# Kernel tuning notes

Hardware: AMD Instinct MI355X
Metric: run time of the kernel (lower is better)

Reference implementation:

```python
import jax, jax.numpy as jnp
from jax import lax
import numpy as np

DEPTH = 4
D_MODEL = 192
D_INNER = 384
D_STATE = 16
D_CONV = 4
DT_RANK = 12
STRIDE = 4
NUM_PATCHES = 400
L_SEQ = NUM_PATCHES + 1  # +1 cls token appended at the end
EPS = 1e-5


def _rmsnorm(x, w):
    x = x.astype(jnp.float32)
    return (x * lax.rsqrt(jnp.mean(x * x, axis=-1, keepdims=True) + EPS)) * w


def _mamba(x, in_w, cw, cb, xp_w, dtw, dtb, A_log, Dv, ow):
    # x: [B, L, D_MODEL]
    B = x.shape[0]
    xz = jnp.einsum('bld,ed->ble', x, in_w)            # [B, L, 2*D_INNER]
    u, z = jnp.split(xz, 2, axis=-1)                   # [B, L, D_INNER] each
    # causal depthwise conv over L
    u_t = jnp.transpose(u, (0, 2, 1))                  # [B, D_INNER, L]
    u_pad = jnp.pad(u_t, ((0, 0), (0, 0), (D_CONV - 1, 0)))
    conv = lax.conv_general_dilated(
        u_pad, cw[:, None, :], (1,), 'VALID',
        dimension_numbers=('NCH', 'OIH', 'NCH'),
        feature_group_count=D_INNER)                   # [B, D_INNER, L]
    u = jax.nn.silu(conv + cb[:, None])
    u = jnp.transpose(u, (0, 2, 1))                    # [B, L, D_INNER]
    xdbl = jnp.einsum('bld,ed->ble', u, xp_w)          # [B, L, 44]
    dt, Bm, Cm = jnp.split(xdbl, [DT_RANK, DT_RANK + D_STATE], axis=-1)
    dt = jax.nn.softplus(jnp.einsum('blr,dr->bld', dt, dtw) + dtb)  # [B, L, D_INNER]
    A = -jnp.exp(A_log)                                # [D_INNER, D_STATE]
    dA = jnp.exp(dt[..., None] * A)                    # [B, L, D_INNER, D_STATE]
    dBu = dt[..., None] * Bm[:, :, None, :] * u[..., None]
    h0 = jnp.zeros((B, D_INNER, D_STATE), dtype=dA.dtype)

    def step(h, inp):
        dA_t, dBu_t = inp
        h = dA_t * h + dBu_t
        return h, h

    _, hs = lax.scan(step, h0, (jnp.swapaxes(dA, 0, 1), jnp.swapaxes(dBu, 0, 1)))
    hs = jnp.swapaxes(hs, 0, 1)                        # [B, L, D_INNER, D_STATE]
    y = jnp.einsum('bldn,bln->bld', hs, Cm) + u * Dv
    y = y * jax.nn.silu(z)
    return jnp.einsum('bld,ed->ble', y, ow)            # [B, L, D_MODEL]


def _forward(imgs, patch_w, patch_b, pos_embed, cls_token, norm_w, in_proj_w,
             conv_w, conv_b, xproj_w, dt_w, dt_b, A_log, D_param, out_w,
             normf_w, head_w, head_b):
    B = imgs.shape[0]
    # StrideEmbed: non-overlapping strides of 4 bytes -> linear to embed_dim
    x = imgs.reshape(B, NUM_PATCHES, STRIDE) @ patch_w + patch_b  # [B, 400, 192]
    x = x + pos_embed[:, :-1, :]
    cls = cls_token + pos_embed[:, -1:, :]             # [1, 1, 192]
    x = jnp.concatenate([x, jnp.broadcast_to(cls, (B, 1, D_MODEL))], axis=1)
    hidden = x
    residual = None
    for i in range(DEPTH):
        residual = hidden if residual is None else hidden + residual  # fp32 residual stream
        h = _rmsnorm(residual, norm_w[i])
        hidden = _mamba(h, in_proj_w[i], conv_w[i], conv_b[i], xproj_w[i],
                        dt_w[i], dt_b[i], A_log[i], D_param[i], out_w[i])
    x = _rmsnorm(hidden + residual, normf_w)
    cls_out = x[:, -1, :]                              # [B, 192]
    logits = cls_out @ head_w.T + head_b               # [B, 1000]
    return logits


def setup_inputs() -> dict:
    key = jax.random.key(0)
    ks = jax.random.split(key, 16)
    B = 32
    rn = lambda k, s, sc: jax.random.normal(k, s, dtype=jnp.float32) * sc
    A_log = jnp.broadcast_to(jnp.log(jnp.arange(1.0, D_STATE + 1.0, dtype=jnp.float32)),
                             (DEPTH, D_INNER, D_STATE))
    return {
        'imgs': rn(ks[0], (B, 1, 40, 40), 1.0),
        'patch_w': rn(ks[1], (STRIDE, D_MODEL), 0.1),
        'patch_b': jnp.zeros((D_MODEL,), jnp.float32),
        'pos_embed': rn(ks[2], (1, L_SEQ, D_MODEL), 0.02),
        'cls_token': rn(ks[3], (1, 1, D_MODEL), 0.02),
        'norm_w': jnp.ones((DEPTH, D_MODEL), jnp.float32),
        'in_proj_w': rn(ks[4], (DEPTH, 2 * D_INNER, D_MODEL), 0.05),
        'conv_w': rn(ks[5], (DEPTH, D_INNER, D_CONV), 0.3),
        'conv_b': jnp.zeros((DEPTH, D_INNER), jnp.float32),
        'xproj_w': rn(ks[6], (DEPTH, DT_RANK + 2 * D_STATE, D_INNER), 0.05),
        'dt_w': rn(ks[7], (DEPTH, D_INNER, DT_RANK), 0.1),
        'dt_b': rn(ks[8], (DEPTH, D_INNER), 0.5) - 4.0,
        'A_log': A_log,
        'D_param': jnp.ones((DEPTH, D_INNER), jnp.float32),
        'out_w': rn(ks[9], (DEPTH, D_MODEL, D_INNER), 0.05),
        'normf_w': jnp.ones((D_MODEL,), jnp.float32),
        'head_w': rn(ks[10], (1000, D_MODEL), 0.05),
        'head_b': jnp.zeros((1000,), jnp.float32),
    }


def reference(imgs, patch_w, patch_b, pos_embed, cls_token, norm_w, in_proj_w,
              conv_w, conv_b, xproj_w, dt_w, dt_b, A_log, D_param, out_w,
              normf_w, head_w, head_b):
    return _forward(imgs, patch_w, patch_b, pos_embed, cls_token, norm_w,
                    in_proj_w, conv_w, conv_b, xproj_w, dt_w, dt_b, A_log,
                    D_param, out_w, normf_w, head_w, head_b)
```

## Files before the change

### kernel.cpp

```cpp
#include <hip/hip_runtime.h>
#include <hip/hip_bf16.h>

#define B_SZ 32
#define LSEQ 401
#define NT (B_SZ * LSEQ)
#define DM 192
#define DI 384
#define DS 16
#define EPSF 1e-5f
#define ST 40
#define STP 44
#define NCH 8
#define PQN 1376256

typedef __attribute__((ext_vector_type(8))) short short8;
typedef __attribute__((ext_vector_type(4))) float f32x4;
typedef __hip_bfloat16 bf16;

#define OFF_IMGS    0
#define OFF_PATCHW  51200
#define OFF_PATCHB  51968
#define OFF_POS     52160
#define OFF_CLS     129152
#define OFF_NORMW   129344
#define OFF_INW     130112
#define OFF_CONVW   719936
#define OFF_CONVB   726080
#define OFF_XPROJW  727616
#define OFF_DTW     795200
#define OFF_DTB     813632
#define OFF_ALOG    815168
#define OFF_DP      839744
#define OFF_OUTW    841280
#define OFF_NORMF   1136192
#define OFF_HEADW   1136384
#define OFF_HEADB   1328384
#define OFF_TOTAL   1329384

#define WB_INW   0
#define WB_XPJ   589824
#define WB_OUT   688128
#define WB_DTW   983040
#define WB_TOTAL 1032192

__device__ __forceinline__ int chunk_s(int c) { return c == 0 ? 0 : c * 50 + 1; }
__device__ __forceinline__ int chunk_e(int c) { return (c + 1) * 50 + 1; }

__device__ __forceinline__ float ldsrc(const void* p, int off, int isbf) {
  return isbf ? __bfloat162float(((const bf16*)p)[off]) : ((const float*)p)[off];
}
__device__ __forceinline__ float fast_silu(float z) {
  return z * __builtin_amdgcn_rcpf(1.f + __expf(-z));
}
__device__ __forceinline__ float fast_softplus(float x) {
  float e = __expf(x);
  return (x > 15.f) ? x : __logf(1.f + e);
}

#define DPP_ADD(x, ctrl) \
  x += __int_as_float(__builtin_amdgcn_update_dpp(0, __float_as_int(x), ctrl, 0xF, 0xF, true))
__device__ __forceinline__ float row_sum16(float x) {
  DPP_ADD(x, 0xB1);
  DPP_ADD(x, 0x4E);
  DPP_ADD(x, 0x124);
  DPP_ADD(x, 0x128);
  return x;
}

struct P18 { const void* p[18]; };

__global__ __launch_bounds__(256) void k_convwb(P18 t, float* __restrict__ fin,
                                                bf16* __restrict__ wb) {
  static const int st[19] = {OFF_IMGS, OFF_PATCHW, OFF_PATCHB, OFF_POS, OFF_CLS,
                             OFF_NORMW, OFF_INW, OFF_CONVW, OFF_CONVB, OFF_XPROJW,
                             OFF_DTW, OFF_DTB, OFF_ALOG, OFF_DP, OFF_OUTW,
                             OFF_NORMF, OFF_HEADW, OFF_HEADB, OFF_TOTAL};
  int isbf = (((const unsigned short*)t.p[5])[0] == 0x3F80) ? 1 : 0;
  int idx = blockIdx.x * 256 + threadIdx.x;
  if (idx < OFF_TOTAL) {
    int lo = 0;
#pragma unroll
    for (int i = 1; i < 18; ++i) if (idx >= st[i]) lo = i;
    fin[idx] = ldsrc(t.p[lo], idx - st[lo], isbf);
  } else if (idx < OFF_TOTAL + WB_TOTAL) {
    int j = idx - OFF_TOTAL;
    float v;
    if (j < WB_XPJ) {
      v = ldsrc(t.p[6], j, isbf);
    } else if (j < WB_OUT) {
      int i2 = j - WB_XPJ;
      int l = i2 / (64 * 384);
      int r = (i2 / 384) & 63;
      int k = i2 % 384;
      v = (r < 44) ? ldsrc(t.p[9], l * 44 * 384 + r * 384 + k, isbf) : 0.f;
    } else if (j < WB_DTW) {
      v = ldsrc(t.p[14], j - WB_OUT, isbf);
    } else {
      int i2 = j - WB_DTW;
      int l = i2 / (384 * 32);
      int r = i2 % (384 * 32);
      int d = r >> 5;
      int k = r & 31;
      v = (k < 12) ? ldsrc(t.p[10], l * 4608 + d * 12 + k, isbf) : 0.f;
    }
    wb[j] = __float2bfloat16(v);
  }
}

__device__ __forceinline__ void inproj32(const bf16 (*shb)[200],
                                         const bf16* __restrict__ Win,
                                         bf16* __restrict__ xb,
                                         bf16* __restrict__ zb,
                                         int row0, int tid) {
  int lane = tid & 63, wave = tid >> 6;
  int q = lane >> 4, mlo = lane & 15;
  short8 afrA[6], afrB[6];
#pragma unroll
  for (int kk = 0; kk < 6; ++kk) {
    afrA[kk] = *(const short8*)&shb[mlo][kk * 32 + q * 8];
    afrB[kk] = *(const short8*)&shb[16 + mlo][kk * 32 + q * 8];
  }
  const bf16* wbase = Win + (size_t)(wave * 96 + mlo) * DM + q * 8;
#pragma unroll
  for (int jh = 0; jh < 2; ++jh) {
    short8 Bb[18];
#pragma unroll
    for (int j = 0; j < 3; ++j)
#pragma unroll
      for (int kk = 0; kk < 6; ++kk)
        Bb[j * 6 + kk] = *(const short8*)(wbase + (size_t)(jh * 3 + j) * 16 * DM + kk * 32);
#pragma unroll
    for (int j = 0; j < 3; ++j) {
      f32x4 aA = {}, aB = {};
#pragma unroll
      for (int kk = 0; kk < 6; ++kk) {
        aA = __builtin_amdgcn_mfma_f32_16x16x32_bf16(afrA[kk], Bb[j * 6 + kk], aA, 0, 0, 0);
        aB = __builtin_amdgcn_mfma_f32_16x16x32_bf16(afrB[kk], Bb[j * 6 + kk], aB, 0, 0, 0);
      }
      int n = wave * 96 + (jh * 3 + j) * 16 + mlo;
      if (n < DI) {
#pragma unroll
        for (int i = 0; i < 4; ++i) {
          xb[(size_t)(row0 + q * 4 + i) * DI + n] = __float2bfloat16(aA[i]);
          xb[(size_t)(row0 + 16 + q * 4 + i) * DI + n] = __float2bfloat16(aB[i]);
        }
      } else {
        int nz = n - DI;
#pragma unroll
        for (int i = 0; i < 4; ++i) {
          zb[(size_t)(row0 + q * 4 + i) * DI + nz] = __float2bfloat16(aA[i]);
          zb[(size_t)(row0 + 16 + q * 4 + i) * DI + nz] = __float2bfloat16(aB[i]);
        }
      }
    }
  }
}

__global__ __launch_bounds__(512)
__attribute__((amdgpu_waves_per_eu(2, 2)))
void k_embedin(const float* __restrict__ fin,
               float* __restrict__ residual,
               const bf16* __restrict__ Win,
               bf16* __restrict__ xb,
               bf16* __restrict__ zb) {
  __shared__ bf16 shb[32][200];
  const float* imgs = fin + OFF_IMGS;
  const float* pw   = fin + OFF_PATCHW;
  const float* pb   = fin + OFF_PATCHB;
  const float* pos  = fin + OFF_POS;
  const float* cls  = fin + OFF_CLS;
  const float* nw0  = fin + OFF_NORMW;
  int tid = threadIdx.x;
  int row0 = blockIdx.x * 32;
  {
    int row = tid >> 4, g = tid & 15;
    int t = row0 + row;
    int b = t / LSEQ, l = t % LSEQ;
    float im[4];
    if (l < 400) {
#pragma unroll
      for (int s = 0; s < 4; ++s) im[s] = imgs[b * 1600 + l * 4 + s];
    }
    float rn[12], ss = 0.f;
#pragma unroll
    for (int k = 0; k < 12; ++k) {
      int col = g + 16 * k;
      float v;
      if (l < 400) {
        v = pb[col] + pos[l * DM + col];
#pragma unroll
        for (int s = 0; s < 4; ++s) v = fmaf(im[s], pw[s * DM + col], v);
      } else {
        v = cls[col] + pos[400 * DM + col];
      }
      residual[(size_t)t * DM + col] = v;
      rn[k] = v;
      ss = fmaf(v, v, ss);
    }
    ss = row_sum16(ss);
    float sres = rsqrtf(ss / (float)DM + EPSF);
#pragma unroll
    for (int k = 0; k < 12; ++k) {
      int col = g + 16 * k;
      shb[row][col] = __float2bfloat16(rn[k] * sres * nw0[col]);
    }
  }
  __syncthreads();
  inproj32(shb, Win, xb, zb, row0, tid);
}

__global__ __launch_bounds__(512) void k_xdt(const bf16* __restrict__ xb,
                                             const float* __restrict__ cw,
                                             const float* __restrict__ cb,
                                             const bf16* __restrict__ Wbf,
                                             float* __restrict__ xdbl,
                                             const bf16* __restrict__ dtwb,
                                             const float* __restrict__ dtb,
                                             bf16* __restrict__ ub,
                                             bf16* __restrict__ dto) {
  __shared__ bf16  sxt[19][392];
  __shared__ bf16  su[16][392];
  __shared__ float4 scw4[384];
  __shared__ float scb[384];
  __shared__ float sxp[2][16][48];
  __shared__ bf16  sxb[16][32];
  int row0 = blockIdx.x * 16;
  int tid = threadIdx.x;
  for (int i = tid; i < 19 * 48; i += 512) {
    int r = i / 48, c8 = i - r * 48;
    int t = row0 - 3 + r;
    if (t < 0) t = 0;
    *(short8*)&sxt[r][c8 * 8] = *(const short8*)(xb + (size_t)t * DI + c8 * 8);
  }
  for (int i = tid; i < 384; i += 512) {
    scw4[i] = ((const float4*)cw)[i];
    scb[i] = cb[i];
  }
  __syncthreads();
  for (int i = tid; i < 768; i += 512) {
    int tok = i / 48;
    int c8 = i - tok * 48;
    int d0 = c8 * 8;
    int t = row0 + tok;
    int l = t % LSEQ;
    float xr[4][8];
#pragma unroll
    for (int k = 0; k < 4; ++k) {
      short8 v = *(const short8*)&sxt[tok + k][d0];
      bool ok = (l - 3 + k) >= 0;
#pragma unroll
      for (int j = 0; j < 8; ++j) {
        unsigned int uu = ((unsigned int)(unsigned short)v[j]) << 16;
        xr[k][j] = ok ? __uint_as_float(uu) : 0.f;
      }
    }
    short8 uvv;
#pragma unroll
    for (int j = 0; j < 8; ++j) {
      float4 w = scw4[d0 + j];
      float a = scb[d0 + j];
      a = fmaf(xr[0][j], w.x, a);
      a = fmaf(xr[1][j], w.y, a);
      a = fmaf(xr[2][j], w.z, a);
      a = fmaf(xr[3][j], w.w, a);
      bf16 h = __float2bfloat16(fast_silu(a));
      uvv[j] = *reinterpret_cast<short*>(&h);
    }
    *(short8*)&su[tok][d0] = uvv;
    *(short8*)(ub + (size_t)t * DI + d0) = uvv;
  }
  __syncthreads();
  int lane = tid & 63;
  int wave = tid >> 6;
  int q = lane >> 4;
  int mlo = lane & 15;
  if (wave < 6) {
    int colw = (wave % 3) * 16;
    int kh = wave / 3;
    f32x4 acc = {};
    for (int k0 = 0; k0 < 192; k0 += 32) {
      short8 a = *(const short8*)&su[mlo][kh * 192 + k0 + q * 8];
      short8 b = *(const short8*)(Wbf + (size_t)(colw + mlo) * DI + kh * 192 + k0 + q * 8);
      acc = __builtin_amdgcn_mfma_f32_16x16x32_bf16(a, b, acc, 0, 0, 0);
    }
#pragma unroll
    for (int i = 0; i < 4; ++i) sxp[kh][q * 4 + i][colw + mlo] = acc[i];
  }
  __syncthreads();
  for (int i = tid; i < 16 * 44; i += 512) {
    int r = i / 44, c = i - r * 44;
    xdbl[(size_t)(row0 + r) * 44 + c] = sxp[0][r][c] + sxp[1][r][c];
  }
  for (int i = tid; i < 512; i += 512) {
    int tok = i >> 5, k = i & 31;
    sxb[tok][k] = __float2bfloat16(k < 12 ? sxp[0][tok][k] + sxp[1][tok][k] : 0.f);
  }
  __syncthreads();
  short8 afrag = *(const short8*)&sxb[mlo][q * 8];
#pragma unroll
  for (int jt = 0; jt < 3; ++jt) {
    int d = (wave * 3 + jt) * 16 + mlo;
    short8 bfrag = *(const short8*)(dtwb + (size_t)d * 32 + q * 8);
    f32x4 acc = {};
    acc = __builtin_amdgcn_mfma_f32_16x16x32_bf16(afrag, bfrag, acc, 0, 0, 0);
    float dtbv = dtb[d];
#pragma unroll
    for (int i = 0; i < 4; ++i)
      dto[(size_t)(row0 + q * 4 + i) * DI + d] =
          __float2bfloat16(fast_softplus(acc[i] + dtbv));
  }
}

__global__ __launch_bounds__(512) void k_scanA(const bf16* __restrict__ ub,
                                               const bf16* __restrict__ dtv,
                                               const float* __restrict__ xdbl,
                                               const float* __restrict__ A_log,
                                               float* __restrict__ Pq) {
  __shared__ float sdt[32][STP], sw[32][STP], sB[16][STP];
  int bx = blockIdx.x, b = blockIdx.y, c = blockIdx.z;
  int d0 = bx * 32;
  int tid = threadIdx.x;
  int dloc = tid >> 4, n = tid & 15;
  float A = -__expf(A_log[(d0 + dloc) * DS + n]);
  float S = 0.f, h = 0.f;
  int base = b * LSEQ;
  int lt = tid >> 5, lj = tid & 31;
  int s = chunk_s(c), e = chunk_e(c);
  for (int t0 = s; t0 < e; t0 += ST) {
    int tc = min(ST, e - t0);
    for (int tt = lt; tt < tc; tt += 16) {
      int g = base + t0 + tt;
      float dv = __bfloat162float(dtv[(size_t)g * DI + d0 + lj]);
      sdt[lj][tt] = dv;
      sw[lj][tt] = dv * __bfloat162float(ub[(size_t)g * DI + d0 + lj]);
      if (lj < 16) sB[lj][tt] = xdbl[(size_t)g * 44 + 12 + lj];
    }
    __syncthreads();
    int l4 = 0;
    for (; l4 + 4 <= tc; l4 += 4) {
      float4 dt4 = *(const float4*)&sdt[dloc][l4];
      float4 w4  = *(const float4*)&sw[dloc][l4];
      float4 B4  = *(const float4*)&sB[n][l4];
      h = fmaf(__expf(dt4.x * A), h, w4.x * B4.x);
      h = fmaf(__expf(dt4.y * A), h, w4.y * B4.y);
      h = fmaf(__expf(dt4.z * A), h, w4.z * B4.z);
      h = fmaf(__expf(dt4.w * A), h, w4.w * B4.w);
      S += dt4.x + dt4.y + dt4.z + dt4.w;
    }
    for (; l4 < tc; ++l4) {
      float dv = sdt[dloc][l4];
      h = fmaf(__expf(dv * A), h, sw[dloc][l4] * sB[n][l4]);
      S += dv;
    }
    __syncthreads();
  }
  int idx = ((c * B_SZ + b) * 12 + bx) * 512 + tid;
  Pq[idx] = __expf(A * S);
  Pq[PQN + idx] = h;
}

__global__ __launch_bounds__(512) void k_scanB(const bf16* __restrict__ zb,
                                               const bf16* __restrict__ ub,
                                               const bf16* __restrict__ dtv,
                                               const float* __restrict__ xdbl,
                                               const float* __restrict__ A_log,
                                               const float* __restrict__ Dp,
                                               const float* __restrict__ Pq,
                                               bf16* __restrict__ yb) {
  __shared__ float sdt[32][STP], sw[32][STP], sB[16][STP], sC[16][STP],
                   sz[32][STP], sy[32][STP];
  int bx = blockIdx.x, b = blockIdx.y, c = blockIdx.z;
  int d0 = bx * 32;
  int tid = threadIdx.x;
  int dloc = tid >> 4, n = tid & 15;
  float A = -__expf(A_log[(d0 + dloc) * DS + n]);
  float h = 0.f;
  for (int j = 0; j < c; ++j) {
    int idx = ((j * B_SZ + b) * 12 + bx) * 512 + tid;
    h = Pq[PQN + idx] + Pq[idx] * h;
  }
  int base = b * LSEQ;
  int lt = tid >> 5, lj = tid & 31;
  float Dvj = Dp[d0 + lj];
  int s = chunk_s(c), e = chunk_e(c);
  for (int t0 = s; t0 < e; t0 += ST) {
    int tc = min(ST, e - t0);
    for (int tt = lt; tt < tc; tt += 16) {
      int g = base + t0 + tt;
      float dv = __bfloat162float(dtv[(size_t)g * DI + d0 + lj]);
      float uv = __bfloat162float(ub[(size_t)g * DI + d0 + lj]);
      sdt[lj][tt] = dv;
      sw[lj][tt] = dv * uv;
      sy[lj][tt] = uv * Dvj;
      sz[lj][tt] = fast_silu(__bfloat162float(zb[(size_t)g * DI + d0 + lj]));
      if (lj < 32) {
        float v = xdbl[(size_t)g * 44 + 12 + lj];
        if (lj < 16) sB[lj][tt] = v;
        else         sC[lj - 16][tt] = v;
      }
    }
    __syncthreads();
    int l4 = 0;
    for (; l4 + 4 <= tc; l4 += 4) {
      float4 dt4 = *(const float4*)&sdt[dloc][l4];
      float4 w4  = *(const float4*)&sw[dloc][l4];
      float4 B4  = *(const float4*)&sB[n][l4];
      float4 C4  = *(const float4*)&sC[n][l4];
      float c0, c1, c2, c3;
      h = fmaf(__expf(dt4.x * A), h, w4.x * B4.x); c0 = row_sum16(h * C4.x);
      h = fmaf(__expf(dt4.y * A), h, w4.y * B4.y); c1 = row_sum16(h * C4.y);
      h = fmaf(__expf(dt4.z * A), h, w4.z * B4.z); c2 = row_sum16(h * C4.z);
      h = fmaf(__expf(dt4.w * A), h, w4.w * B4.w); c3 = row_sum16(h * C4.w);
      if (n == 0) {
        float4 uD4 = *(const float4*)&sy[dloc][l4];
        float4 z4  = *(const float4*)&sz[dloc][l4];
        float4 yv;
        yv.x = (c0 + uD4.x) * z4.x;
        yv.y = (c1 + uD4.y) * z4.y;
        yv.z = (c2 + uD4.z) * z4.z;
        yv.w = (c3 + uD4.w) * z4.w;
        *(float4*)&sy[dloc][l4] = yv;
      }
    }
    for (; l4 < tc; ++l4) {
      h = fmaf(__expf(sdt[dloc][l4] * A), h, sw[dloc][l4] * sB[n][l4]);
      float cc = row_sum16(h * sC[n][l4]);
      if (n == 0) sy[dloc][l4] = (cc + sy[dloc][l4]) * sz[dloc][l4];
    }
    __syncthreads();
    for (int tt = lt; tt < tc; tt += 16)
      yb[(size_t)(base + t0 + tt) * DI + d0 + lj] = __float2bfloat16(sy[lj][tt]);
    __syncthreads();
  }
}

__global__ __launch_bounds__(512)
__attribute__((amdgpu_waves_per_eu(2, 2)))
void k_outin(const bf16* __restrict__ yb,
             const bf16* __restrict__ Wout,
             float* __restrict__ residual,
             const float* __restrict__ nw,
             const bf16* __restrict__ Win,
             bf16* __restrict__ xb,
             bf16* __restrict__ zb) {
  __shared__ bf16  syt[32][392];
  __shared__ float sCt[2][32][200];
  __shared__ bf16  shb[32][200];
  int tid = threadIdx.x;
  int lane = tid & 63;
  int wave = tid >> 6;
  int row0 = blockIdx.x * 32;
  int q = lane >> 4;
  int mlo = lane & 15;
  {
    int i0 = tid, i1 = tid + 512, i2 = tid + 1024;
    const bf16* src = yb + (size_t)row0 * DI;
    short8 v0 = *(const short8*)(src + (i0 / 48) * DI + (i0 % 48) * 8);
    short8 v1 = *(const short8*)(src + (i1 / 48) * DI + (i1 % 48) * 8);
    short8 v2 = *(const short8*)(src + (i2 / 48) * DI + (i2 % 48) * 8);
    *(short8*)&syt[i0 / 48][(i0 % 48) * 8] = v0;
    *(short8*)&syt[i1 / 48][(i1 % 48) * 8] = v1;
    *(short8*)&syt[i2 / 48][(i2 % 48) * 8] = v2;
  }
  __syncthreads();
  {
    int colw = (wave & 3) * 48;
    int kh = wave >> 2;
    const bf16* brow = Wout + (size_t)(colw + mlo) * DI + kh * 192 + q * 8;
    short8 Bf[18];
#pragma unroll
    for (int j = 0; j < 3; ++j)
#pragma unroll
      for (int k2 = 0; k2 < 6; ++k2)
        Bf[j * 6 + k2] = *(const short8*)(brow + (size_t)j * 16 * DI + k2 * 32);
    short8 afA[6], afB[6];
#pragma unroll
    for (int k2 = 0; k2 < 6; ++k2) {
      afA[k2] = *(const short8*)&syt[mlo][kh * 192 + k2 * 32 + q * 8];
      afB[k2] = *(const short8*)&syt[16 + mlo][kh * 192 + k2 * 32 + q * 8];
    }
    f32x4 acc[2][3] = {};
#pragma unroll
    for (int k2 = 0; k2 < 6; ++k2) {
#pragma unroll
      for (int j = 0; j < 3; ++j) {
        acc[0][j] = __builtin_amdgcn_mfma_f32_16x16x32_bf16(afA[k2], Bf[j * 6 + k2], acc[0][j], 0, 0, 0);
        acc[1][j] = __builtin_amdgcn_mfma_f32_16x16x32_bf16(afB[k2], Bf[j * 6 + k2], acc[1][j], 0, 0, 0);
      }
    }
#pragma unroll
    for (int rg = 0; rg < 2; ++rg)
#pragma unroll
      for (int j = 0; j < 3; ++j)
#pragma unroll
        for (int i = 0; i < 4; ++i)
          sCt[kh][rg * 16 + q * 4 + i][colw + j * 16 + mlo] = acc[rg][j][i];
  }
  __syncthreads();
  {
    int row = tid >> 4, g = tid & 15;
    int t = row0 + row;
    float* rp = residual + (size_t)t * DM + g * 12;
    float4 r4[3];
#pragma unroll
    for (int j = 0; j < 3; ++j) r4[j] = *(const float4*)(rp + j * 4);
    float rn[12], ss = 0.f;
#pragma unroll
    for (int k = 0; k < 12; ++k) {
      int col = g * 12 + k;
      float x = sCt[0][row][col] + sCt[1][row][col] + ((const float*)r4)[k];
      rn[k] = x;
      ss = fmaf(x, x, ss);
    }
    ss = row_sum16(ss);
    float sres = rsqrtf(ss / (float)DM + EPSF);
#pragma unroll
    for (int j = 0; j < 3; ++j) {
      float4 w4;
      w4.x = rn[j * 4 + 0]; w4.y = rn[j * 4 + 1];
      w4.z = rn[j * 4 + 2]; w4.w = rn[j * 4 + 3];
      *(float4*)(rp + j * 4) = w4;
    }
#pragma unroll
    for (int k = 0; k < 12; ++k) {
      int col = g * 12 + k;
      shb[row][col] = __float2bfloat16(rn[k] * sres * nw[col]);
    }
  }
  __syncthreads();
  inproj32(shb, Win, xb, zb, row0, tid);
}

__global__ __launch_bounds__(256) void k_lastout(const bf16* __restrict__ yb,
                                                 const bf16* __restrict__ Wout,
                                                 const float* __restrict__ resIn,
                                                 float* __restrict__ clsbuf) {
  __shared__ float sCt[16][200];
  int tid = threadIdx.x;
  int lane = tid & 63;
  int wave = tid >> 6;
  int b0 = blockIdx.x * 16;
  int q = lane >> 4;
  int mlo = lane & 15;
  int colw = wave * 48;
  f32x4 acc[3] = {};
  const bf16* arow = yb + ((size_t)(b0 + mlo) * LSEQ + 400) * DI + q * 8;
  for (int k0 = 0; k0 < DI; k0 += 32) {
    short8 a = *(const short8*)(arow + k0);
#pragma unroll
    for (int j = 0; j < 3; ++j) {
      short8 b = *(const short8*)(Wout + (size_t)(colw + j * 16 + mlo) * DI + k0 + q * 8);
      acc[j] = __builtin_amdgcn_mfma_f32_16x16x32_bf16(a, b, acc[j], 0, 0, 0);
    }
  }
#pragma unroll
  for (int j = 0; j < 3; ++j)
#pragma unroll
    for (int i = 0; i < 4; ++i) sCt[q * 4 + i][colw + j * 16 + mlo] = acc[j][i];
  __syncthreads();
  int row = tid >> 4, g = tid & 15;
  int bb = b0 + row;
#pragma unroll
  for (int k = 0; k < 12; ++k) {
    int col = g + 16 * k;
    clsbuf[(size_t)bb * DM + col] =
        sCt[row][col] + resIn[((size_t)bb * LSEQ + 400) * DM + col];
  }
}

__global__ __launch_bounds__(256) void k_final(const float* __restrict__ clsbuf,
                                               const float* __restrict__ fin,
                                               const void* __restrict__ nw_raw,
                                               void* __restrict__ out) {
  const float* normf  = fin + OFF_NORMF;
  const float* head_w = fin + OFF_HEADW;
  const float* head_b = fin + OFF_HEADB;
  __shared__ float clsv[DM];
  __shared__ float partial[4];
  __shared__ float sres;
  int b = blockIdx.x;
  float r = 0.f;
  if (threadIdx.x < DM) r = clsbuf[(size_t)b * DM + threadIdx.x];
  float ss = r * r;
#pragma unroll
  for (int m = 32; m >= 1; m >>= 1) ss += __shfl_xor(ss, m, 64);
  if ((threadIdx.x & 63) == 0) partial[threadIdx.x >> 6] = ss;
  __syncthreads();
  if (threadIdx.x == 0)
    sres = rsqrtf((partial[0] + partial[1] + partial[2] + partial[3]) / (float)DM + EPSF);
  __syncthreads();
  if (threadIdx.x < DM) clsv[threadIdx.x] = r * sres * normf[threadIdx.x];
  __syncthreads();
  int isbf = (((const unsigned short*)nw_raw)[0] == 0x3F80) ? 1 : 0;
  for (int e = threadIdx.x; e < 1000; e += 256) {
    float acc = head_b[e];
    for (int k = 0; k < DM; ++k) acc = fmaf(clsv[k], head_w[e * DM + k], acc);
    if (isbf) ((bf16*)out)[b * 1000 + e] = __float2bfloat16(acc);
    else      ((float*)out)[b * 1000 + e] = acc;
  }
}

extern "C" void kernel_launch(void* const* d_in, const int* in_sizes, int n_in,
                              void* d_out, int out_size, void* d_ws, size_t ws_size,
                              hipStream_t stream) {
  char* base = (char*)d_ws;
  size_t off = 0;
  auto alloc = [&](size_t bytes) { char* p = base + off; off = (off + bytes + 255) & ~(size_t)255; return p; };
  float* fin      = (float*)alloc((size_t)OFF_TOTAL * 4);
  bf16*  wb       = (bf16*)alloc((size_t)WB_TOTAL * 2);
  float* residual = (float*)alloc((size_t)NT * DM * 4);
  bf16*  xb       = (bf16*)alloc((size_t)NT * DI * 2);
  bf16*  zb       = (bf16*)alloc((size_t)NT * DI * 2);
  bf16*  ub       = (bf16*)alloc((size_t)NT * DI * 2);
  float* xdbl     = (float*)alloc((size_t)NT * 44 * 4);
  bf16*  dtb16    = (bf16*)alloc((size_t)NT * DI * 2);
  float* Pq       = (float*)alloc((size_t)2 * PQN * 4);
  float* clsbuf   = (float*)alloc((size_t)B_SZ * DM * 4);
  bf16*  yb       = ub;

  P18 t;
  for (int i = 0; i < 18; ++i) t.p[i] = d_in[i];
  k_convwb<<<(OFF_TOTAL + WB_TOTAL + 255) / 256, 256, 0, stream>>>(t, fin, wb);

  k_embedin<<<NT / 32, 512, 0, stream>>>(fin, residual, wb + WB_INW, xb, zb);

  for (int layer = 0; layer < 4; ++layer) {
    const float* dtb = fin + OFF_DTB + layer * DI;
    const float* alog = fin + OFF_ALOG + layer * DI * DS;

    k_xdt<<<NT / 16, 512, 0, stream>>>(xb, fin + OFF_CONVW + layer * DI * 4,
                                       fin + OFF_CONVB + layer * DI,
                                       wb + WB_XPJ + layer * 64 * DI, xdbl,
                                       wb + WB_DTW + layer * 384 * 32, dtb, ub, dtb16);

    k_scanA<<<dim3(12, B_SZ, NCH - 1), 512, 0, stream>>>(ub, dtb16, xdbl, alog, Pq);
    k_scanB<<<dim3(12, B_SZ, NCH), 512, 0, stream>>>(zb, ub, dtb16, xdbl, alog,
                                                     fin + OFF_DP + layer * DI, Pq, yb);

    if (layer < 3) {
      k_outin<<<NT / 32, 512, 0, stream>>>(yb, wb + WB_OUT + layer * DM * DI, residual,
                                           fin + OFF_NORMW + (layer + 1) * DM,
                                           wb + WB_INW + (layer + 1) * 768 * DM, xb, zb);
    } else {
      k_lastout<<<2, 256, 0, stream>>>(yb, wb + WB_OUT + 3 * DM * DI, residual, clsbuf);
    }
  }
  k_final<<<B_SZ, 256, 0, stream>>>(clsbuf, fin, d_in[5], d_out);
}
```

Before: 568.9 us.

## Restructure selective scan: per-thread channel with 16 states, more chunks, separate prefix kernel

```diff
diff --git a/kernel.cpp b/kernel.cpp
--- a/kernel.cpp
+++ b/kernel.cpp
@@ -8,10 +8,7 @@
 #define DI 384
 #define DS 16
 #define EPSF 1e-5f
-#define ST 40
-#define STP 44
-#define NCH 8
-#define PQN 1376256
+#define NCH 16
 
 typedef __attribute__((ext_vector_type(8))) short short8;
 typedef __attribute__((ext_vector_type(4))) float f32x4;
@@ -43,8 +40,8 @@
 #define WB_DTW   983040
 #define WB_TOTAL 1032192
 
-__device__ __forceinline__ int chunk_s(int c) { return c == 0 ? 0 : c * 50 + 1; }
-__device__ __forceinline__ int chunk_e(int c) { return (c + 1) * 50 + 1; }
+__device__ __forceinline__ int chunk_s(int c) { return c == 0 ? 0 : 25 * c + 1; }
+__device__ __forceinline__ int chunk_e(int c) { return 25 * c + 26; }
 
 __device__ __forceinline__ float ldsrc(const void* p, int off, int isbf) {
   return isbf ? __bfloat162float(((const bf16*)p)[off]) : ((const float*)p)[off];
@@ -55,6 +52,9 @@
 __device__ __forceinline__ float fast_softplus(float x) {
   float e = __expf(x);
   return (x > 15.f) ? x : __logf(1.f + e);
+}
+__device__ __forceinline__ float bfbits(unsigned short u) {
+  return __uint_as_float(((unsigned int)u) << 16);
 }
 
 #define DPP_ADD(x, ctrl) \
@@ -311,126 +311,155 @@
   }
 }
 
-__global__ __launch_bounds__(512) void k_scanA(const bf16* __restrict__ ub,
-                                               const bf16* __restrict__ dtv,
-                                               const float* __restrict__ xdbl,
-                                               const float* __restrict__ A_log,
-                                               float* __restrict__ Pq) {
-  __shared__ float sdt[32][STP], sw[32][STP], sB[16][STP];
-  int bx = blockIdx.x, b = blockIdx.y, c = blockIdx.z;
-  int d0 = bx * 32;
-  int tid = threadIdx.x;
-  int dloc = tid >> 4, n = tid & 15;
-  float A = -__expf(A_log[(d0 + dloc) * DS + n]);
-  float S = 0.f, h = 0.f;
+__global__ __launch_bounds__(384)
+__attribute__((amdgpu_waves_per_eu(2, 2)))
+void k_scanA(const bf16* __restrict__ ub,
+             const bf16* __restrict__ dtv,
+             const float* __restrict__ xdbl,
+             const float* __restrict__ A_log,
+             float* __restrict__ Sq,
+             float* __restrict__ Hq) {
+  __shared__ float sB[26][16];
+  int cc = blockIdx.x, b = blockIdx.y;
+  int d = threadIdx.x;
+  int s = chunk_s(cc), tc = chunk_e(cc) - s;
   int base = b * LSEQ;
-  int lt = tid >> 5, lj = tid & 31;
-  int s = chunk_s(c), e = chunk_e(c);
-  for (int t0 = s; t0 < e; t0 += ST) {
-    int tc = min(ST, e - t0);
-    for (int tt = lt; tt < tc; tt += 16) {
-      int g = base + t0 + tt;
-      float dv = __bfloat162float(dtv[(size_t)g * DI + d0 + lj]);
-      sdt[lj][tt] = dv;
-      sw[lj][tt] = dv * __bfloat162float(ub[(size_t)g * DI + d0 + lj]);
-      if (lj < 16) sB[lj][tt] = xdbl[(size_t)g * 44 + 12 + lj];
-    }
-    __syncthreads();
-    int l4 = 0;
-    for (; l4 + 4 <= tc; l4 += 4) {
-      float4 dt4 = *(const float4*)&sdt[dloc][l4];
-      float4 w4  = *(const float4*)&sw[dloc][l4];
-      float4 B4  = *(const float4*)&sB[n][l4];
-      h = fmaf(__expf(dt4.x * A), h, w4.x * B4.x);
-      h = fmaf(__expf(dt4.y * A), h, w4.y * B4.y);
-      h = fmaf(__expf(dt4.z * A), h, w4.z * B4.z);
-      h = fmaf(__expf(dt4.w * A), h, w4.w * B4.w);
-      S += dt4.x + dt4.y + dt4.z + dt4.w;
-    }
-    for (; l4 < tc; ++l4) {
-      float dv = sdt[dloc][l4];
-      h = fmaf(__expf(dv * A), h, sw[dloc][l4] * sB[n][l4]);
-      S += dv;
-    }
-    __syncthreads();
-  }
-  int idx = ((c * B_SZ + b) * 12 + bx) * 512 + tid;
-  Pq[idx] = __expf(A * S);
-  Pq[PQN + idx] = h;
-}
-
-__global__ __launch_bounds__(512) void k_scanB(const bf16* __restrict__ zb,
-                                               const bf16* __restrict__ ub,
-                                               const bf16* __restrict__ dtv,
-                                               const float* __restrict__ xdbl,
-                                               const float* __restrict__ A_log,
-                                               const float* __restrict__ Dp,
-                                               const float* __restrict__ Pq,
-                                               bf16* __restrict__ yb) {
-  __shared__ float sdt[32][STP], sw[32][STP], sB[16][STP], sC[16][STP],
-                   sz[32][STP], sy[32][STP];
-  int bx = blockIdx.x, b = blockIdx.y, c = blockIdx.z;
-  int d0 = bx * 32;
-  int tid = threadIdx.x;
-  int dloc = tid >> 4, n = tid & 15;
-  float A = -__expf(A_log[(d0 + dloc) * DS + n]);
-  float h = 0.f;
-  for (int j = 0; j < c; ++j) {
-    int idx = ((j * B_SZ + b) * 12 + bx) * 512 + tid;
-    h = Pq[PQN + idx] + Pq[idx] * h;
-  }
+  for (int i = d; i < tc * 16; i += 384) {
+    int t = i >> 4, col = i & 15;
+    sB[t][col] = xdbl[(size_t)(base + s + t) * 44 + 12 + col];
+  }
+  __syncthreads();
+  float A[16], h[16];
+#pragma unroll
+  for (int j = 0; j < 4; ++j) {
+    f32x4 al = *(const f32x4*)&A_log[d * DS + j * 4];
+#pragma unroll
+    for (int i = 0; i < 4; ++i) { A[j * 4 + i] = -__expf(al[i]); h[j * 4 + i] = 0.f; }
+  }
+  float S = 0.f;
+  const unsigned short* pd = (const unsigned short*)(dtv + (size_t)(base + s) * DI + d);
+  const unsigned short* pu = (const unsigned short*)(ub  + (size_t)(base + s) * DI + d);
+  unsigned short dN = *pd, uN = *pu;
+  for (int t = 0; t < tc; ++t) {
+    unsigned short dC = dN, uC = uN;
+    if (t + 1 < tc) { pd += DI; pu += DI; dN = *pd; uN = *pu; }
+    float dv = bfbits(dC), uv = bfbits(uC);
+    float w = dv * uv;
+    S += dv;
+    f32x4 B0 = *(const f32x4*)&sB[t][0];
+    f32x4 B1 = *(const f32x4*)&sB[t][4];
+    f32x4 B2 = *(const f32x4*)&sB[t][8];
+    f32x4 B3 = *(const f32x4*)&sB[t][12];
+#pragma unroll
+    for (int n = 0; n < 16; ++n) {
+      float Bn = (n < 4) ? B0[n] : (n < 8) ? B1[n - 4] : (n < 12) ? B2[n - 8] : B3[n - 12];
+      float E = __expf(dv * A[n]);
+      h[n] = fmaf(E, h[n], w * Bn);
+    }
+  }
+  size_t si = ((size_t)cc * B_SZ + b) * 384 + d;
+  Sq[si] = S;
+#pragma unroll
+  for (int j = 0; j < 4; ++j) {
+    f32x4 hv;
+#pragma unroll
+    for (int i = 0; i < 4; ++i) hv[i] = h[j * 4 + i];
+    *(f32x4*)&Hq[si * 16 + j * 4] = hv;
+  }
+}
+
+__global__ __launch_bounds__(256) void k_scanP(const float* __restrict__ A_log,
+                                               const float* __restrict__ Sq,
+                                               float* __restrict__ Hq) {
+  int idx = blockIdx.x * 256 + threadIdx.x;
+  int n = idx & 15;
+  int dd = (idx >> 4) % 384;
+  int b = idx / (384 * 16);
+  float A = -__expf(A_log[dd * DS + n]);
+  float hs = 0.f;
+  for (int c = 0; c < NCH - 1; ++c) {
+    size_t si = ((size_t)c * B_SZ + b) * 384 + dd;
+    float P = __expf(A * Sq[si]);
+    size_t hi = si * 16 + n;
+    float he = Hq[hi];
+    hs = fmaf(P, hs, he);
+    Hq[hi] = hs;
+  }
+}
+
+__global__ __launch_bounds__(384)
+__attribute__((amdgpu_waves_per_eu(2, 2)))
+void k_scanB(const bf16* __restrict__ zb,
+             const bf16* __restrict__ ub,
+             const bf16* __restrict__ dtv,
+             const float* __restrict__ xdbl,
+             const float* __restrict__ A_log,
+             const float* __restrict__ Dp,
+             const float* __restrict__ Hq,
+             bf16* __restrict__ yb) {
+  __shared__ float sB[26][16], sC[26][16];
+  int cc = blockIdx.x, b = blockIdx.y;
+  int d = threadIdx.x;
+  int s = chunk_s(cc), tc = chunk_e(cc) - s;
   int base = b * LSEQ;
-  int lt = tid >> 5, lj = tid & 31;
-  float Dvj = Dp[d0 + lj];
-  int s = chunk_s(c), e = chunk_e(c);
-  for (int t0 = s; t0 < e; t0 += ST) {
-    int tc = min(ST, e - t0);
-    for (int tt = lt; tt < tc; tt += 16) {
-      int g = base + t0 + tt;
-      float dv = __bfloat162float(dtv[(size_t)g * DI + d0 + lj]);
-      float uv = __bfloat162float(ub[(size_t)g * DI + d0 + lj]);
-      sdt[lj][tt] = dv;
-      sw[lj][tt] = dv * uv;
-      sy[lj][tt] = uv * Dvj;
-      sz[lj][tt] = fast_silu(__bfloat162float(zb[(size_t)g * DI + d0 + lj]));
-      if (lj < 32) {
-        float v = xdbl[(size_t)g * 44 + 12 + lj];
-        if (lj < 16) sB[lj][tt] = v;
-        else         sC[lj - 16][tt] = v;
-      }
-    }
-    __syncthreads();
-    int l4 = 0;
-    for (; l4 + 4 <= tc; l4 += 4) {
-      float4 dt4 = *(const float4*)&sdt[dloc][l4];
-      float4 w4  = *(const float4*)&sw[dloc][l4];
-      float4 B4  = *(const float4*)&sB[n][l4];
-      float4 C4  = *(const float4*)&sC[n][l4];
-      float c0, c1, c2, c3;
-      h = fmaf(__expf(dt4.x * A), h, w4.x * B4.x); c0 = row_sum16(h * C4.x);
-      h = fmaf(__expf(dt4.y * A), h, w4.y * B4.y); c1 = row_sum16(h * C4.y);
-      h = fmaf(__expf(dt4.z * A), h, w4.z * B4.z); c2 = row_sum16(h * C4.z);
-      h = fmaf(__expf(dt4.w * A), h, w4.w * B4.w); c3 = row_sum16(h * C4.w);
-      if (n == 0) {
-        float4 uD4 = *(const float4*)&sy[dloc][l4];
-        float4 z4  = *(const float4*)&sz[dloc][l4];
-        float4 yv;
-        yv.x = (c0 + uD4.x) * z4.x;
-        yv.y = (c1 + uD4.y) * z4.y;
-        yv.z = (c2 + uD4.z) * z4.z;
-        yv.w = (c3 + uD4.w) * z4.w;
-        *(float4*)&sy[dloc][l4] = yv;
-      }
-    }
-    for (; l4 < tc; ++l4) {
-      h = fmaf(__expf(sdt[dloc][l4] * A), h, sw[dloc][l4] * sB[n][l4]);
-      float cc = row_sum16(h * sC[n][l4]);
-      if (n == 0) sy[dloc][l4] = (cc + sy[dloc][l4]) * sz[dloc][l4];
-    }
-    __syncthreads();
-    for (int tt = lt; tt < tc; tt += 16)
-      yb[(size_t)(base + t0 + tt) * DI + d0 + lj] = __float2bfloat16(sy[lj][tt]);
-    __syncthreads();
+  for (int i = d; i < tc * 32; i += 384) {
+    int t = i >> 5, col = i & 31;
+    float v = xdbl[(size_t)(base + s + t) * 44 + 12 + col];
+    if (col < 16) sB[t][col] = v;
+    else          sC[t][col - 16] = v;
+  }
+  __syncthreads();
+  float A[16], h[16];
+#pragma unroll
+  for (int j = 0; j < 4; ++j) {
+    f32x4 al = *(const f32x4*)&A_log[d * DS + j * 4];
+#pragma unroll
+    for (int i = 0; i < 4; ++i) A[j * 4 + i] = -__expf(al[i]);
+  }
+  if (cc == 0) {
+#pragma unroll
+    for (int n = 0; n < 16; ++n) h[n] = 0.f;
+  } else {
+    size_t hi = (((size_t)(cc - 1) * B_SZ + b) * 384 + d) * 16;
+#pragma unroll
+    for (int j = 0; j < 4; ++j) {
+      f32x4 hv = *(const f32x4*)&Hq[hi + j * 4];
+#pragma unroll
+      for (int i = 0; i < 4; ++i) h[j * 4 + i] = hv[i];
+    }
+  }
+  float Dv = Dp[d];
+  const unsigned short* pd = (const unsigned short*)(dtv + (size_t)(base + s) * DI + d);
+  const unsigned short* pu = (const unsigned short*)(ub  + (size_t)(base + s) * DI + d);
+  const unsigned short* pz = (const unsigned short*)(zb  + (size_t)(base + s) * DI + d);
+  bf16* py = yb + (size_t)(base + s) * DI + d;
+  unsigned short dN = *pd, uN = *pu, zN = *pz;
+  for (int t = 0; t < tc; ++t) {
+    unsigned short dC = dN, uC = uN, zC = zN;
+    if (t + 1 < tc) { pd += DI; pu += DI; pz += DI; dN = *pd; uN = *pu; zN = *pz; }
+    float dv = bfbits(dC), uv = bfbits(uC), zv = bfbits(zC);
+    float w = dv * uv;
+    f32x4 B0 = *(const f32x4*)&sB[t][0];
+    f32x4 B1 = *(const f32x4*)&sB[t][4];
+    f32x4 B2 = *(const f32x4*)&sB[t][8];
+    f32x4 B3 = *(const f32x4*)&sB[t][12];
+    f32x4 C0 = *(const f32x4*)&sC[t][0];
+    f32x4 C1 = *(const f32x4*)&sC[t][4];
+    f32x4 C2 = *(const f32x4*)&sC[t][8];
+    f32x4 C3 = *(const f32x4*)&sC[t][12];
+    float y0 = 0.f, y1 = 0.f;
+#pragma unroll
+    for (int n = 0; n < 16; ++n) {
+      float Bn = (n < 4) ? B0[n] : (n < 8) ? B1[n - 4] : (n < 12) ? B2[n - 8] : B3[n - 12];
+      float Cn = (n < 4) ? C0[n] : (n < 8) ? C1[n - 4] : (n < 12) ? C2[n - 8] : C3[n - 12];
+      float E = __expf(dv * A[n]);
+      h[n] = fmaf(E, h[n], w * Bn);
+      if (n & 1) y1 = fmaf(h[n], Cn, y1);
+      else       y0 = fmaf(h[n], Cn, y0);
+    }
+    float yv = (y0 + y1 + uv * Dv) * fast_silu(zv);
+    *py = __float2bfloat16(yv);
+    py += DI;
   }
 }
 
@@ -614,7 +643,8 @@
   bf16*  ub       = (bf16*)alloc((size_t)NT * DI * 2);
   float* xdbl     = (float*)alloc((size_t)NT * 44 * 4);
   bf16*  dtb16    = (bf16*)alloc((size_t)NT * DI * 2);
-  float* Pq       = (float*)alloc((size_t)2 * PQN * 4);
+  float* Sq       = (float*)alloc((size_t)(NCH - 1) * B_SZ * 384 * 4);
+  float* Hq       = (float*)alloc((size_t)(NCH - 1) * B_SZ * 384 * 16 * 4);
   float* clsbuf   = (float*)alloc((size_t)B_SZ * DM * 4);
   bf16*  yb       = ub;
 
@@ -633,9 +663,10 @@
                                        wb + WB_XPJ + layer * 64 * DI, xdbl,
                                        wb + WB_DTW + layer * 384 * 32, dtb, ub, dtb16);
 
-    k_scanA<<<dim3(12, B_SZ, NCH - 1), 512, 0, stream>>>(ub, dtb16, xdbl, alog, Pq);
-    k_scanB<<<dim3(12, B_SZ, NCH), 512, 0, stream>>>(zb, ub, dtb16, xdbl, alog,
-                                                     fin + OFF_DP + layer * DI, Pq, yb);
+    k_scanA<<<dim3(NCH - 1, B_SZ), 384, 0, stream>>>(ub, dtb16, xdbl, alog, Sq, Hq);
+    k_scanP<<<(B_SZ * 384 * 16) / 256, 256, 0, stream>>>(alog, Sq, Hq);
+    k_scanB<<<dim3(NCH, B_SZ), 384, 0, stream>>>(zb, ub, dtb16, xdbl, alog,
+                                                 fin + OFF_DP + layer * DI, Hq, yb);
 
     if (layer < 3) {
       k_outin<<<NT / 32, 512, 0, stream>>>(yb, wb + WB_OUT + layer * DM * DI, residual,
```

New measurement: 594.9 us. 4.6% more time.
